# Kernel optimization log

Measured on AMD Instinct MI355X. Metric: run time of the kernel, lower is better.

## Reference

```python
import jax, jax.numpy as jnp
import numpy as np

IN_IM_SZ = 224   # network input size (in_im_sz)
OUT = 7          # RoIAlign output size (out_size)
SCALE = 1.0 / 16.0  # spatial scale feature/input


def _roi_align_one(feat, boxes):
    # feat: [C, Hf, Wf]; boxes: [P, 4] in network-input coords (x1,y1,x2,y2)
    C, H, W = feat.shape
    b = boxes * SCALE
    x1, y1, x2, y2 = b[:, 0], b[:, 1], b[:, 2], b[:, 3]
    bw = (x2 - x1) / OUT
    bh = (y2 - y1) / OUT
    off = jnp.arange(OUT, dtype=feat.dtype) + 0.5
    xs = x1[:, None] + off[None, :] * bw[:, None]   # [P, OUT]
    ys = y1[:, None] + off[None, :] * bh[:, None]   # [P, OUT]
    P = boxes.shape[0]
    X = jnp.broadcast_to(jnp.clip(xs[:, None, :], 0.0, W - 1), (P, OUT, OUT))
    Y = jnp.broadcast_to(jnp.clip(ys[:, :, None], 0.0, H - 1), (P, OUT, OUT))
    x0 = jnp.clip(jnp.floor(X).astype(jnp.int32), 0, W - 1)
    y0 = jnp.clip(jnp.floor(Y).astype(jnp.int32), 0, H - 1)
    x1i = jnp.minimum(x0 + 1, W - 1)
    y1i = jnp.minimum(y0 + 1, H - 1)
    lx = X - x0
    ly = Y - y0
    # gathers: [C, P, OUT, OUT]
    f00 = feat[:, y0, x0]
    f01 = feat[:, y0, x1i]
    f10 = feat[:, y1i, x0]
    f11 = feat[:, y1i, x1i]
    val = (f00 * (1 - ly) * (1 - lx) + f01 * (1 - ly) * lx
           + f10 * ly * (1 - lx) + f11 * ly * lx)
    return jnp.transpose(val, (1, 0, 2, 3))  # [P, C, OUT, OUT]


_roi_align = jax.vmap(_roi_align_one)  # [B,C,H,W],[B,P,4] -> [B,P,C,OUT,OUT]


def setup_inputs() -> dict:
    key = jax.random.key(0)
    ks = jax.random.split(key, 12)
    B, NH, NO, C, HF = 4, 16, 16, 1024, 14
    im_h, im_w = 480, 640
    features = jax.random.normal(ks[0], (B, C, HF, HF), jnp.float32)

    def make_boxes(k1, k2, k3, k4, k5, n, cls):
        x1 = jax.random.uniform(k1, (B, n)) * (im_w * 0.5)
        y1 = jax.random.uniform(k2, (B, n)) * (im_h * 0.5)
        w = 20.0 + jax.random.uniform(k3, (B, n)) * (im_w * 0.4)
        h = 20.0 + jax.random.uniform(k4, (B, n)) * (im_h * 0.4)
        x2 = jnp.minimum(x1 + w, im_w - 1.0)
        y2 = jnp.minimum(y1 + h, im_h - 1.0)
        score = jax.random.uniform(k5, (B, n))
        return jnp.stack([x1, y1, x2, y2, score, cls], axis=-1).astype(jnp.float32)

    H_Box = make_boxes(ks[1], ks[2], ks[3], ks[4], ks[5], NH,
                       jnp.ones((B, NH)))  # class 1 = person
    o_cls = jax.random.randint(ks[11], (B, NO), 1, 19).astype(jnp.float32)
    O_Box = make_boxes(ks[6], ks[7], ks[8], ks[9], ks[10], NO, o_cls)
    return {"features": features, "H_Box": H_Box, "O_Box": O_Box,
            "im_h": im_h, "im_w": im_w}


def reference(features, H_Box, O_Box, im_h, im_w):
    B, NH = H_Box.shape[:2]
    NO = O_Box.shape[1]
    C = features.shape[1]
    rW = IN_IM_SZ / float(im_w)
    rH = IN_IM_SZ / float(im_h)
    sc = jnp.array([rW, rH, rW, rH], features.dtype)

    # per-box RoIAlign (human / object nodes)
    H_Node = _roi_align(features, H_Box[..., :4] * sc)  # [B,NH,C,7,7]
    O_Node = _roi_align(features, O_Box[..., :4] * sc)  # [B,NO,C,7,7]

    # pairwise union boxes (image coords), as in H_O_BBOX
    h4 = H_Box[:, :, None, :4]  # [B,NH,1,4]
    o4 = O_Box[:, None, :, :4]  # [B,1,NO,4]
    ux1 = jnp.minimum(o4[..., 0], h4[..., 0])
    uy1 = jnp.minimum(o4[..., 1], h4[..., 1])
    ux2 = jnp.maximum(o4[..., 2], h4[..., 2])
    uy2 = jnp.maximum(o4[..., 3], h4[..., 3])
    U = jnp.stack([ux1, uy1, ux2, uy2], axis=-1)  # [B,NH,NO,4]
    H_O_Node = _roi_align(features, (U * sc).reshape(B, NH * NO, 4))
    H_O_Node = H_O_Node.reshape(B, NH, NO, C, OUT, OUT)

    # geometry encoding (box_encode), vectorized over all pairs
    hx1, hy1, hx2, hy2 = [h4[..., i] for i in range(4)]  # [B,NH,1]
    ox1, oy1, ox2, oy2 = [o4[..., i] for i in range(4)]  # [B,1,NO]
    h_cx, h_cy = (hx1 + hx2) / 2, (hy1 + hy2) / 2
    h_w, h_h = hx2 - hx1, hy2 - hy1
    o_cx, o_cy = (ox1 + ox2) / 2, (oy1 + oy2) / 2
    o_w, o_h = ox2 - ox1, oy2 - oy1
    dxc = h_cx - o_cx
    dyc = h_cy - o_cy
    d_x = jnp.abs(dxc) / h_w * 100.0
    d_y = jnp.abs(dyc) / h_h * 100.0
    d_xy = jnp.sqrt(dxc ** 2 + dyc ** 2) / (h_w + h_h) * 100.0
    dx_ratio = jnp.abs(dxc) / im_w * 100.0
    dy_ratio = jnp.abs(dyc) / im_h * 100.0
    det_y = jnp.where(jnp.abs(dyc) > 1e-5, dyc,
                      jnp.where(dyc > 0, 1e-5, -1e-5))
    angle = jnp.arctan(dxc / det_y)
    area_scale = (o_w * o_h) / (h_w * h_h)
    o_scale = o_h / o_w
    ix1 = jnp.maximum(hx1, ox1)
    iy1 = jnp.maximum(hy1, oy1)
    ix2 = jnp.minimum(hx2, ox2)
    iy2 = jnp.minimum(hy2, oy2)
    inter = jnp.maximum(ix2 - ix1, 0.0) * jnp.maximum(iy2 - iy1, 0.0)
    union = h_w * h_h + o_w * o_h - inter
    iou = jnp.where(inter > 0, inter / union, 0.0)
    geometry = jnp.stack(
        [jnp.broadcast_to(t, (B, NH, NO)) for t in
         (d_x, d_y, d_xy, dx_ratio, dy_ratio, angle, area_scale, o_scale, iou)],
        axis=-1)  # [B,NH,NO,9]

    # area_sacale_ratio for H, O and union boxes
    im_area = float(im_h) * float(im_w)
    h_ratio = (H_Box[..., 2] - H_Box[..., 0]) * (H_Box[..., 3] - H_Box[..., 1]) / im_area * 100.0
    o_ratio = (O_Box[..., 2] - O_Box[..., 0]) * (O_Box[..., 3] - O_Box[..., 1]) / im_area * 100.0
    ho_ratio = (ux2 - ux1) * (uy2 - uy1) / im_area * 100.0

    return (H_Node, O_Node, H_O_Node, geometry, h_ratio, o_ratio, ho_ratio)
```

## Files before the change

kernel.cpp:

```cpp
#include <hip/hip_runtime.h>


#define C_CH   1024
#define HW     14
#define PLANE  196
#define OUTS   7
#define TILE   (C_CH * OUTS * OUTS)
#define OFF_O  3211264
#define OFF_U  6422528
#define OFF_G  57802752
#define OFF_HR 57811968
#define OFF_OR 57812032
#define OFF_UR 57812096

#define CH_PER_BLK   16
#define ROI_PER_BLK  16
#define CH_PER_WAVE  4

#define BXS    (CH_PER_BLK * PLANE)

__global__ __launch_bounds__(256, 8) void roi_align_kernel(
    const float* __restrict__ feat,
    const float* __restrict__ HBox,
    const float* __restrict__ OBox,
    const int* __restrict__ im_h_p,
    const int* __restrict__ im_w_p,
    float* __restrict__ out)
{
    __shared__ float lds[BXS + 192];

    const float im_w = (float)(*im_w_p);
    const float im_h = (float)(*im_h_p);

    if (blockIdx.y == 72) {
        if (blockIdx.x >= 4) return;
        const int p = blockIdx.x * 256 + threadIdx.x;
        const float im_area = im_h * im_w;

        const int b = p >> 8;
        const int h = (p >> 4) & 15;
        const int o = p & 15;
        const float* hb = HBox + (b * 16 + h) * 6;
        const float* ob = OBox + (b * 16 + o) * 6;
        const float hx1 = hb[0], hy1 = hb[1], hx2 = hb[2], hy2 = hb[3];
        const float ox1 = ob[0], oy1 = ob[1], ox2 = ob[2], oy2 = ob[3];

        const float h_cx = (hx1 + hx2) * 0.5f, h_cy = (hy1 + hy2) * 0.5f;
        const float h_w = hx2 - hx1, h_h = hy2 - hy1;
        const float o_cx = (ox1 + ox2) * 0.5f, o_cy = (oy1 + oy2) * 0.5f;
        const float o_w = ox2 - ox1, o_h = oy2 - oy1;

        const float dxc = h_cx - o_cx;
        const float dyc = h_cy - o_cy;
        const float adx = fabsf(dxc), ady = fabsf(dyc);

        const float d_x = adx / h_w * 100.0f;
        const float d_y = ady / h_h * 100.0f;
        const float d_xy = sqrtf(dxc * dxc + dyc * dyc) / (h_w + h_h) * 100.0f;
        const float dx_ratio = adx / im_w * 100.0f;
        const float dy_ratio = ady / im_h * 100.0f;
        const float det_y = (ady > 1e-5f) ? dyc : ((dyc > 0.0f) ? 1e-5f : -1e-5f);
        const float angle = atanf(dxc / det_y);
        const float area_scale = (o_w * o_h) / (h_w * h_h);
        const float o_scale = o_h / o_w;

        const float ix1 = fmaxf(hx1, ox1), iy1 = fmaxf(hy1, oy1);
        const float ix2 = fminf(hx2, ox2), iy2 = fminf(hy2, oy2);
        const float inter = fmaxf(ix2 - ix1, 0.0f) * fmaxf(iy2 - iy1, 0.0f);
        const float uni = h_w * h_h + o_w * o_h - inter;
        const float iou = (inter > 0.0f) ? inter / uni : 0.0f;

        float* g = out + OFF_G + (size_t)p * 9;
        g[0] = d_x; g[1] = d_y; g[2] = d_xy;
        g[3] = dx_ratio; g[4] = dy_ratio; g[5] = angle;
        g[6] = area_scale; g[7] = o_scale; g[8] = iou;

        const float ux1 = fminf(ox1, hx1), uy1 = fminf(oy1, hy1);
        const float ux2 = fmaxf(ox2, hx2), uy2 = fmaxf(oy2, hy2);
        out[OFF_UR + p] = (ux2 - ux1) * (uy2 - uy1) / im_area * 100.0f;

        if (p < 64) {
            const float* hb2 = HBox + p * 6;
            out[OFF_HR + p] = (hb2[2] - hb2[0]) * (hb2[3] - hb2[1]) / im_area * 100.0f;
            const float* ob2 = OBox + p * 6;
            out[OFF_OR + p] = (ob2[2] - ob2[0]) * (ob2[3] - ob2[1]) / im_area * 100.0f;
        }
        return;
    }

    const int c0 = blockIdx.x * CH_PER_BLK;
    const int g0 = blockIdx.y * ROI_PER_BLK;
    const int b  = g0 / 288;

    {
        const float4* g4 = (const float4*)(feat + ((size_t)b * C_CH + c0) * PLANE);
        float4* l4 = (float4*)lds;
        for (int i = threadIdx.x; i < (CH_PER_BLK * PLANE / 4); i += 256)
            l4[i] = g4[i];
    }
    if (threadIdx.x < 96)
        lds[BXS + threadIdx.x] = HBox[b * 96 + threadIdx.x];
    else if (threadIdx.x < 192)
        lds[BXS + threadIdx.x] = OBox[b * 96 + (threadIdx.x - 96)];
    __syncthreads();

    const int lane = threadIdx.x & 63;
    const int wave = threadIdx.x >> 6;
    if (lane >= 49) return;

    const int pos = lane;
    const int oy = pos / 7;
    const int ox = pos - oy * 7;

    const float scx = (224.0f / im_w) * (1.0f / 16.0f);
    const float scy = (224.0f / im_h) * (1.0f / 16.0f);

    const float* ldw = lds + (wave * CH_PER_WAVE) * PLANE;
    const int cw = c0 + wave * CH_PER_WAVE;

    const float* hbx = lds + BXS;
    const float* obx = lds + BXS + 96;

    for (int ri = 0; ri < ROI_PER_BLK; ++ri) {
        const int g = g0 + ri;
        const int j = g - b * 288;

        float x1, y1, x2, y2;
        size_t outBase;
        if (j < 16) {
            const float* bx = hbx + j * 6;
            x1 = bx[0]; y1 = bx[1]; x2 = bx[2]; y2 = bx[3];
            outBase = (size_t)(b * 16 + j) * TILE;
        } else if (j < 32) {
            const float* bx = obx + (j - 16) * 6;
            x1 = bx[0]; y1 = bx[1]; x2 = bx[2]; y2 = bx[3];
            outBase = OFF_O + (size_t)(b * 16 + (j - 16)) * TILE;
        } else {
            const int u = j - 32;
            const float* hb = hbx + (u >> 4) * 6;
            const float* ob = obx + (u & 15) * 6;
            x1 = fminf(ob[0], hb[0]);
            y1 = fminf(ob[1], hb[1]);
            x2 = fmaxf(ob[2], hb[2]);
            y2 = fmaxf(ob[3], hb[3]);
            outBase = OFF_U + (size_t)(b * 256 + u) * TILE;
        }

        const float bx1 = x1 * scx;
        const float by1 = y1 * scy;
        const float bw = (x2 * scx - bx1) * (1.0f / OUTS);
        const float bh = (y2 * scy - by1) * (1.0f / OUTS);
        float X = bx1 + ((float)ox + 0.5f) * bw;
        float Y = by1 + ((float)oy + 0.5f) * bh;
        X = fminf(fmaxf(X, 0.0f), (float)(HW - 1));
        Y = fminf(fmaxf(Y, 0.0f), (float)(HW - 1));
        const int x0 = min((int)floorf(X), HW - 2);
        const int y0 = min((int)floorf(Y), HW - 2);
        const float lx = X - (float)x0;
        const float ly = Y - (float)y0;
        const float w00 = (1.0f - ly) * (1.0f - lx);
        const float w01 = (1.0f - ly) * lx;
        const float w10 = ly * (1.0f - lx);
        const float w11 = ly * lx;
        const int off = y0 * HW + x0;

        const float* lp = ldw + off;
        float* op = out + outBase + (size_t)cw * 49 + pos;
#pragma unroll
        for (int k = 0; k < CH_PER_WAVE; ++k) {
            const float f00 = lp[0];
            const float f01 = lp[1];
            const float f10 = lp[HW];
            const float f11 = lp[HW + 1];
            op[49 * k] = f00 * w00 + f01 * w01 + f10 * w10 + f11 * w11;
            lp += PLANE;
        }
    }
}

extern "C" void kernel_launch(void* const* d_in, const int* in_sizes, int n_in,
                              void* d_out, int out_size, void* d_ws, size_t ws_size,
                              hipStream_t stream) {
    const float* feat = (const float*)d_in[0];
    const float* HBox = (const float*)d_in[1];
    const float* OBox = (const float*)d_in[2];
    const int* im_h = (const int*)d_in[3];
    const int* im_w = (const int*)d_in[4];
    float* out = (float*)d_out;

    dim3 grid(64, 73);
    roi_align_kernel<<<grid, 256, 0, stream>>>(feat, HBox, OBox, im_h, im_w, out);
}
```

Baseline: 239.9 us.

## Assign one ROI per block and loop over channel chunks staged in LDS

Reorganizes the grid so each block handles a single ROI across all 1024 channels, streaming the batch's features through LDS in 32-channel chunks. Interpolation coordinates and weights are computed once per block instead of once per ROI iteration. The output per block becomes one contiguous 200KB tile. In exchange, every block re-reads the whole feature map for its batch, and the per-chunk barriers leave loads and compute unoverlapped.

```diff
diff --git a/kernel.cpp b/kernel.cpp
--- a/kernel.cpp
+++ b/kernel.cpp
@@ -13,13 +13,11 @@
 #define OFF_OR 57812032
 #define OFF_UR 57812096
 
-#define CH_PER_BLK   16
-#define ROI_PER_BLK  16
-#define CH_PER_WAVE  4
+#define CHUNK       32
+#define NCHUNK      (C_CH / CHUNK)
+#define CH_PER_WAVE (CHUNK / 4)
 
-#define BXS    (CH_PER_BLK * PLANE)
-
-__global__ __launch_bounds__(256, 8) void roi_align_kernel(
+__global__ __launch_bounds__(256, 6) void roi_align_kernel(
     const float* __restrict__ feat,
     const float* __restrict__ HBox,
     const float* __restrict__ OBox,
@@ -27,14 +25,14 @@
     const int* __restrict__ im_w_p,
     float* __restrict__ out)
 {
-    __shared__ float lds[BXS + 192];
+    __shared__ float lds[CHUNK * PLANE];
 
     const float im_w = (float)(*im_w_p);
     const float im_h = (float)(*im_h_p);
+    const int idx = blockIdx.x;
 
-    if (blockIdx.y == 72) {
-        if (blockIdx.x >= 4) return;
-        const int p = blockIdx.x * 256 + threadIdx.x;
+    if (idx >= 1152) {
+        const int p = (idx - 1152) * 256 + threadIdx.x;
         const float im_area = im_h * im_w;
 
         const int b = p >> 8;
@@ -88,26 +86,32 @@
         return;
     }
 
-    const int c0 = blockIdx.x * CH_PER_BLK;
-    const int g0 = blockIdx.y * ROI_PER_BLK;
-    const int b  = g0 / 288;
+    const int b = idx / 288;
+    const int j = idx - b * 288;
 
-    {
-        const float4* g4 = (const float4*)(feat + ((size_t)b * C_CH + c0) * PLANE);
-        float4* l4 = (float4*)lds;
-        for (int i = threadIdx.x; i < (CH_PER_BLK * PLANE / 4); i += 256)
-            l4[i] = g4[i];
+    float x1, y1, x2, y2;
+    size_t outBase;
+    if (j < 16) {
+        const float* bx = HBox + (b * 16 + j) * 6;
+        x1 = bx[0]; y1 = bx[1]; x2 = bx[2]; y2 = bx[3];
+        outBase = (size_t)(b * 16 + j) * TILE;
+    } else if (j < 32) {
+        const float* bx = OBox + (b * 16 + (j - 16)) * 6;
+        x1 = bx[0]; y1 = bx[1]; x2 = bx[2]; y2 = bx[3];
+        outBase = OFF_O + (size_t)(b * 16 + (j - 16)) * TILE;
+    } else {
+        const int u = j - 32;
+        const float* hb = HBox + (b * 16 + (u >> 4)) * 6;
+        const float* ob = OBox + (b * 16 + (u & 15)) * 6;
+        x1 = fminf(ob[0], hb[0]);
+        y1 = fminf(ob[1], hb[1]);
+        x2 = fmaxf(ob[2], hb[2]);
+        y2 = fmaxf(ob[3], hb[3]);
+        outBase = OFF_U + (size_t)(b * 256 + u) * TILE;
     }
-    if (threadIdx.x < 96)
-        lds[BXS + threadIdx.x] = HBox[b * 96 + threadIdx.x];
-    else if (threadIdx.x < 192)
-        lds[BXS + threadIdx.x] = OBox[b * 96 + (threadIdx.x - 96)];
-    __syncthreads();
 
     const int lane = threadIdx.x & 63;
     const int wave = threadIdx.x >> 6;
-    if (lane >= 49) return;
-
     const int pos = lane;
     const int oy = pos / 7;
     const int ox = pos - oy * 7;
@@ -115,66 +119,51 @@
     const float scx = (224.0f / im_w) * (1.0f / 16.0f);
     const float scy = (224.0f / im_h) * (1.0f / 16.0f);
 
-    const float* ldw = lds + (wave * CH_PER_WAVE) * PLANE;
-    const int cw = c0 + wave * CH_PER_WAVE;
+    const float bx1 = x1 * scx;
+    const float by1 = y1 * scy;
+    const float bw = (x2 * scx - bx1) * (1.0f / OUTS);
+    const float bh = (y2 * scy - by1) * (1.0f / OUTS);
+    float X = bx1 + ((float)ox + 0.5f) * bw;
+    float Y = by1 + ((float)oy + 0.5f) * bh;
+    X = fminf(fmaxf(X, 0.0f), (float)(HW - 1));
+    Y = fminf(fmaxf(Y, 0.0f), (float)(HW - 1));
+    const int x0 = min((int)floorf(X), HW - 2);
+    const int y0 = min((int)floorf(Y), HW - 2);
+    const float lx = X - (float)x0;
+    const float ly = Y - (float)y0;
+    const float w00 = (1.0f - ly) * (1.0f - lx);
+    const float w01 = (1.0f - ly) * lx;
+    const float w10 = ly * (1.0f - lx);
+    const float w11 = ly * lx;
+    const int off = y0 * HW + x0;
 
-    const float* hbx = lds + BXS;
-    const float* obx = lds + BXS + 96;
+    const float* feat_b = feat + (size_t)b * C_CH * PLANE;
+    float* outT = out + outBase;
 
-    for (int ri = 0; ri < ROI_PER_BLK; ++ri) {
-        const int g = g0 + ri;
-        const int j = g - b * 288;
+    for (int ch = 0; ch < NCHUNK; ++ch) {
+        {
+            const float4* g4 = (const float4*)(feat_b + (size_t)(ch * CHUNK) * PLANE);
+            float4* l4 = (float4*)lds;
+            for (int i = threadIdx.x; i < (CHUNK * PLANE / 4); i += 256)
+                l4[i] = g4[i];
+        }
+        __syncthreads();
 
-        float x1, y1, x2, y2;
-        size_t outBase;
-        if (j < 16) {
-            const float* bx = hbx + j * 6;
-            x1 = bx[0]; y1 = bx[1]; x2 = bx[2]; y2 = bx[3];
-            outBase = (size_t)(b * 16 + j) * TILE;
-        } else if (j < 32) {
-            const float* bx = obx + (j - 16) * 6;
-            x1 = bx[0]; y1 = bx[1]; x2 = bx[2]; y2 = bx[3];
-            outBase = OFF_O + (size_t)(b * 16 + (j - 16)) * TILE;
-        } else {
-            const int u = j - 32;
-            const float* hb = hbx + (u >> 4) * 6;
-            const float* ob = obx + (u & 15) * 6;
-            x1 = fminf(ob[0], hb[0]);
-            y1 = fminf(ob[1], hb[1]);
-            x2 = fmaxf(ob[2], hb[2]);
-            y2 = fmaxf(ob[3], hb[3]);
-            outBase = OFF_U + (size_t)(b * 256 + u) * TILE;
+        if (lane < 49) {
+            const float* lp = lds + wave * PLANE + off;
+            float* op = outT + (size_t)(ch * CHUNK + wave) * 49 + pos;
+#pragma unroll
+            for (int kk = 0; kk < CH_PER_WAVE; ++kk) {
+                const float f00 = lp[0];
+                const float f01 = lp[1];
+                const float f10 = lp[HW];
+                const float f11 = lp[HW + 1];
+                op[0] = f00 * w00 + f01 * w01 + f10 * w10 + f11 * w11;
+                lp += 4 * PLANE;
+                op += 4 * 49;
+            }
         }
-
-        const float bx1 = x1 * scx;
-        const float by1 = y1 * scy;
-        const float bw = (x2 * scx - bx1) * (1.0f / OUTS);
-        const float bh = (y2 * scy - by1) * (1.0f / OUTS);
-        float X = bx1 + ((float)ox + 0.5f) * bw;
-        float Y = by1 + ((float)oy + 0.5f) * bh;
-        X = fminf(fmaxf(X, 0.0f), (float)(HW - 1));
-        Y = fminf(fmaxf(Y, 0.0f), (float)(HW - 1));
-        const int x0 = min((int)floorf(X), HW - 2);
-        const int y0 = min((int)floorf(Y), HW - 2);
-        const float lx = X - (float)x0;
-        const float ly = Y - (float)y0;
-        const float w00 = (1.0f - ly) * (1.0f - lx);
-        const float w01 = (1.0f - ly) * lx;
-        const float w10 = ly * (1.0f - lx);
-        const float w11 = ly * lx;
-        const int off = y0 * HW + x0;
-
-        const float* lp = ldw + off;
-        float* op = out + outBase + (size_t)cw * 49 + pos;
-#pragma unroll
-        for (int k = 0; k < CH_PER_WAVE; ++k) {
-            const float f00 = lp[0];
-            const float f01 = lp[1];
-            const float f10 = lp[HW];
-            const float f11 = lp[HW + 1];
-            op[49 * k] = f00 * w00 + f01 * w01 + f10 * w10 + f11 * w11;
-            lp += PLANE;
-        }
+        __syncthreads();
     }
 }
 
@@ -188,6 +177,5 @@
     const int* im_w = (const int*)d_in[4];
     float* out = (float*)d_out;
 
-    dim3 grid(64, 73);
-    roi_align_kernel<<<grid, 256, 0, stream>>>(feat, HBox, OBox, im_h, im_w, out);
+    roi_align_kernel<<<1156, 256, 0, stream>>>(feat, HBox, OBox, im_h, im_w, out);
 }
```

New measurement: 350.2 us. 1.46x slower.

## Interleave ROIs across slots and reload feature tiles only on batch change

Applied to the files above, without the earlier changes.

The kernel now gives each block a strided set of 16 ROIs (slot + 72*ri) across all batches and 32 channels. It reloads the channel tile into LDS only when the batch index changes, instead of each block loading its tile once for 16 consecutive ROIs of one batch. Box coordinates are read from global memory rather than staged in LDS, and the launch-bounds occupancy hint is dropped. The intent is to even out the work mix across blocks and halve the number of blocks, at the cost of more tile reloads per block, extra syncs, and twice as much LDS per block.

```diff
diff --git a/kernel.cpp b/kernel.cpp
--- a/kernel.cpp
+++ b/kernel.cpp
@@ -13,13 +13,11 @@
 #define OFF_OR 57812032
 #define OFF_UR 57812096
 
-#define CH_PER_BLK   16
-#define ROI_PER_BLK  16
-#define CH_PER_WAVE  4
+#define CH_PER_BLK   32
+#define CH_PER_WAVE  8
+#define NSLOT        72
 
-#define BXS    (CH_PER_BLK * PLANE)
-
-__global__ __launch_bounds__(256, 8) void roi_align_kernel(
+__global__ __launch_bounds__(256) void roi_align_kernel(
     const float* __restrict__ feat,
     const float* __restrict__ HBox,
     const float* __restrict__ OBox,
@@ -27,14 +25,14 @@
     const int* __restrict__ im_w_p,
     float* __restrict__ out)
 {
-    __shared__ float lds[BXS + 192];
+    __shared__ float lds[CH_PER_BLK * PLANE];
 
     const float im_w = (float)(*im_w_p);
     const float im_h = (float)(*im_h_p);
 
-    if (blockIdx.y == 72) {
-        if (blockIdx.x >= 4) return;
-        const int p = blockIdx.x * 256 + threadIdx.x;
+    if (blockIdx.x == NSLOT) {
+        if (blockIdx.y >= 4) return;
+        const int p = blockIdx.y * 256 + threadIdx.x;
         const float im_area = im_h * im_w;
 
         const int b = p >> 8;
@@ -88,26 +86,11 @@
         return;
     }
 
-    const int c0 = blockIdx.x * CH_PER_BLK;
-    const int g0 = blockIdx.y * ROI_PER_BLK;
-    const int b  = g0 / 288;
-
-    {
-        const float4* g4 = (const float4*)(feat + ((size_t)b * C_CH + c0) * PLANE);
-        float4* l4 = (float4*)lds;
-        for (int i = threadIdx.x; i < (CH_PER_BLK * PLANE / 4); i += 256)
-            l4[i] = g4[i];
-    }
-    if (threadIdx.x < 96)
-        lds[BXS + threadIdx.x] = HBox[b * 96 + threadIdx.x];
-    else if (threadIdx.x < 192)
-        lds[BXS + threadIdx.x] = OBox[b * 96 + (threadIdx.x - 96)];
-    __syncthreads();
+    const int slot = blockIdx.x;
+    const int c0 = blockIdx.y * CH_PER_BLK;
 
     const int lane = threadIdx.x & 63;
     const int wave = threadIdx.x >> 6;
-    if (lane >= 49) return;
-
     const int pos = lane;
     const int oy = pos / 7;
     const int ox = pos - oy * 7;
@@ -118,62 +101,77 @@
     const float* ldw = lds + (wave * CH_PER_WAVE) * PLANE;
     const int cw = c0 + wave * CH_PER_WAVE;
 
-    const float* hbx = lds + BXS;
-    const float* obx = lds + BXS + 96;
+    int cur_b = -1;
 
-    for (int ri = 0; ri < ROI_PER_BLK; ++ri) {
-        const int g = g0 + ri;
-        const int j = g - b * 288;
+    for (int ri = 0; ri < 16; ++ri) {
+        const int t = slot + NSLOT * ri;
 
+        int b;
         float x1, y1, x2, y2;
         size_t outBase;
-        if (j < 16) {
-            const float* bx = hbx + j * 6;
+        if (t < 64) {
+            b = t >> 4;
+            const float* bx = HBox + t * 6;
             x1 = bx[0]; y1 = bx[1]; x2 = bx[2]; y2 = bx[3];
-            outBase = (size_t)(b * 16 + j) * TILE;
-        } else if (j < 32) {
-            const float* bx = obx + (j - 16) * 6;
+            outBase = (size_t)t * TILE;
+        } else if (t < 128) {
+            const int u = t - 64;
+            b = u >> 4;
+            const float* bx = OBox + u * 6;
             x1 = bx[0]; y1 = bx[1]; x2 = bx[2]; y2 = bx[3];
-            outBase = OFF_O + (size_t)(b * 16 + (j - 16)) * TILE;
+            outBase = OFF_O + (size_t)u * TILE;
         } else {
-            const int u = j - 32;
-            const float* hb = hbx + (u >> 4) * 6;
-            const float* ob = obx + (u & 15) * 6;
+            const int u = t - 128;
+            b = u >> 8;
+            const float* hb = HBox + (b * 16 + ((u >> 4) & 15)) * 6;
+            const float* ob = OBox + (b * 16 + (u & 15)) * 6;
             x1 = fminf(ob[0], hb[0]);
             y1 = fminf(ob[1], hb[1]);
             x2 = fmaxf(ob[2], hb[2]);
             y2 = fmaxf(ob[3], hb[3]);
-            outBase = OFF_U + (size_t)(b * 256 + u) * TILE;
+            outBase = OFF_U + (size_t)u * TILE;
         }
 
-        const float bx1 = x1 * scx;
-        const float by1 = y1 * scy;
-        const float bw = (x2 * scx - bx1) * (1.0f / OUTS);
-        const float bh = (y2 * scy - by1) * (1.0f / OUTS);
-        float X = bx1 + ((float)ox + 0.5f) * bw;
-        float Y = by1 + ((float)oy + 0.5f) * bh;
-        X = fminf(fmaxf(X, 0.0f), (float)(HW - 1));
-        Y = fminf(fmaxf(Y, 0.0f), (float)(HW - 1));
-        const int x0 = min((int)floorf(X), HW - 2);
-        const int y0 = min((int)floorf(Y), HW - 2);
-        const float lx = X - (float)x0;
-        const float ly = Y - (float)y0;
-        const float w00 = (1.0f - ly) * (1.0f - lx);
-        const float w01 = (1.0f - ly) * lx;
-        const float w10 = ly * (1.0f - lx);
-        const float w11 = ly * lx;
-        const int off = y0 * HW + x0;
+        if (b != cur_b) {
+            __syncthreads();
+            const float4* g4 = (const float4*)(feat + ((size_t)b * C_CH + c0) * PLANE);
+            float4* l4 = (float4*)lds;
+            for (int i = threadIdx.x; i < (CH_PER_BLK * PLANE / 4); i += 256)
+                l4[i] = g4[i];
+            __syncthreads();
+            cur_b = b;
+        }
 
-        const float* lp = ldw + off;
-        float* op = out + outBase + (size_t)cw * 49 + pos;
+        if (lane < 49) {
+            const float bx1 = x1 * scx;
+            const float by1 = y1 * scy;
+            const float bw = (x2 * scx - bx1) * (1.0f / OUTS);
+            const float bh = (y2 * scy - by1) * (1.0f / OUTS);
+            float X = bx1 + ((float)ox + 0.5f) * bw;
+            float Y = by1 + ((float)oy + 0.5f) * bh;
+            X = fminf(fmaxf(X, 0.0f), (float)(HW - 1));
+            Y = fminf(fmaxf(Y, 0.0f), (float)(HW - 1));
+            const int x0 = min((int)floorf(X), HW - 2);
+            const int y0 = min((int)floorf(Y), HW - 2);
+            const float lx = X - (float)x0;
+            const float ly = Y - (float)y0;
+            const float w00 = (1.0f - ly) * (1.0f - lx);
+            const float w01 = (1.0f - ly) * lx;
+            const float w10 = ly * (1.0f - lx);
+            const float w11 = ly * lx;
+            const int off = y0 * HW + x0;
+
+            const float* lp = ldw + off;
+            float* op = out + outBase + (size_t)cw * 49 + pos;
 #pragma unroll
-        for (int k = 0; k < CH_PER_WAVE; ++k) {
-            const float f00 = lp[0];
-            const float f01 = lp[1];
-            const float f10 = lp[HW];
-            const float f11 = lp[HW + 1];
-            op[49 * k] = f00 * w00 + f01 * w01 + f10 * w10 + f11 * w11;
-            lp += PLANE;
+            for (int k = 0; k < CH_PER_WAVE; ++k) {
+                const float f00 = lp[0];
+                const float f01 = lp[1];
+                const float f10 = lp[HW];
+                const float f11 = lp[HW + 1];
+                op[49 * k] = f00 * w00 + f01 * w01 + f10 * w10 + f11 * w11;
+                lp += PLANE;
+            }
         }
     }
 }
@@ -188,6 +186,6 @@
     const int* im_w = (const int*)d_in[4];
     float* out = (float*)d_out;
 
-    dim3 grid(64, 73);
+    dim3 grid(NSLOT + 1, 32);
     roi_align_kernel<<<grid, 256, 0, stream>>>(feat, HBox, OBox, im_h, im_w, out);
 }
```

After: 245.0 us. 2.2% more time.
